# Kernel optimization log

Hardware: AMD Instinct MI355X
Metric: run time of the kernel (lower is better)

## Reference

```python
import jax, jax.numpy as jnp
import numpy as np

N = 2048      # total nodes across all graphs
G = 16        # number of graphs
IN = 16       # input_dim
D = 256       # hidden_dim (d_model)
NH = 8        # num_heads
HD = D // NH  # head_dim
FF = 4 * D    # dim_feedforward
L = 4         # num_layers
LAT = 32      # latent_dim
BH = D // 2   # beta_head hidden
LN_EPS = 1e-5


def setup_inputs() -> dict:
    key = jax.random.key(0)
    ks = jax.random.split(key, 32)

    def w(k, shape, fan_in):
        return jax.random.normal(k, shape, jnp.float32) * (1.0 / np.sqrt(fan_in))

    inp = {
        "x": jax.random.normal(ks[0], (N, IN), jnp.float32),
        "coords": jax.random.normal(ks[1], (N, 3), jnp.float32),
        "batch": jnp.sort(jax.random.randint(ks[2], (N,), 0, G)).astype(jnp.int32),
        # input projection
        "Wi": w(ks[3], (IN, D), IN), "bi": jnp.zeros((D,), jnp.float32),
        # per-layer transformer params, stacked on leading layer dim
        "qkv_w": w(ks[4], (L, D, 3 * D), D), "qkv_b": jnp.zeros((L, 3 * D), jnp.float32),
        "out_w": w(ks[5], (L, D, D), D),     "out_b": jnp.zeros((L, D), jnp.float32),
        "ff1_w": w(ks[6], (L, D, FF), D),    "ff1_b": jnp.zeros((L, FF), jnp.float32),
        "ff2_w": w(ks[7], (L, FF, D), FF),   "ff2_b": jnp.zeros((L, D), jnp.float32),
        "ln1_s": jnp.ones((L, D), jnp.float32), "ln1_b": jnp.zeros((L, D), jnp.float32),
        "ln2_s": jnp.ones((L, D), jnp.float32), "ln2_b": jnp.zeros((L, D), jnp.float32),
        # heads
        "lat_w": w(ks[8], (D, LAT), D), "lat_b": jnp.zeros((LAT,), jnp.float32),
        "b1_w": w(ks[9], (D, BH), D),   "b1_b": jnp.zeros((BH,), jnp.float32),
        "b2_w": w(ks[10], (BH, 1), BH), "b2_b": jnp.zeros((1,), jnp.float32),
    }
    return inp


def _layer_norm(h, s, b):
    m = jnp.mean(h, axis=-1, keepdims=True)
    v = jnp.mean(jnp.square(h - m), axis=-1, keepdims=True)
    return (h - m) * jax.lax.rsqrt(v + LN_EPS) * s + b


def _forward(x, batch, Wi, bi, qkv_w, qkv_b, out_w, out_b, ff1_w, ff1_b,
             ff2_w, ff2_b, ln1_s, ln1_b, ln2_s, ln2_b, lat_w, lat_b,
             b1_w, b1_b, b2_w, b2_b):
    n = x.shape[0]
    h = x @ Wi + bi  # [N, D]
    # the per-graph python loop in torch == block-diagonal attention mask
    attn_bias = jnp.where(batch[:, None] == batch[None, :], 0.0, -1e9).astype(h.dtype)  # [N, N]
    scale = 1.0 / np.sqrt(HD)
    for l in range(L):
        qkv = h @ qkv_w[l] + qkv_b[l]                 # [N, 3D]
        q, k, v = jnp.split(qkv, 3, axis=-1)
        q = q.reshape(n, NH, HD)
        k = k.reshape(n, NH, HD)
        v = v.reshape(n, NH, HD)
        scores = jnp.einsum('nhd,mhd->hnm', q, k) * scale + attn_bias[None]  # [H, N, N]
        a = jax.nn.softmax(scores, axis=-1)
        o = jnp.einsum('hnm,mhd->nhd', a, v).reshape(n, D)
        o = o @ out_w[l] + out_b[l]
        h = _layer_norm(h + o, ln1_s[l], ln1_b[l])     # post-norm (torch default)
        f = jax.nn.relu(h @ ff1_w[l] + ff1_b[l]) @ ff2_w[l] + ff2_b[l]
        h = _layer_norm(h + f, ln2_s[l], ln2_b[l])
    lat = h @ lat_w + lat_b                            # [N, LAT]
    norm = jnp.maximum(jnp.linalg.norm(lat, axis=-1, keepdims=True), 1e-12)
    lat = lat / norm * np.sqrt(LAT)
    beta = jax.nn.sigmoid(jax.nn.relu(h @ b1_w + b1_b) @ b2_w + b2_b)  # [N, 1]
    beta = jnp.clip(beta, 1e-6, 1.0 - 1e-6)
    return beta, lat


def reference(x, coords, batch, Wi, bi, qkv_w, qkv_b, out_w, out_b,
              ff1_w, ff1_b, ff2_w, ff2_b, ln1_s, ln1_b, ln2_s, ln2_b,
              lat_w, lat_b, b1_w, b1_b, b2_w, b2_b):
    # coords is accepted (signature fidelity) but unused in the original forward
    del coords
    return _forward(x, batch, Wi, bi, qkv_w, qkv_b, out_w, out_b, ff1_w, ff1_b,
                    ff2_w, ff2_b, ln1_s, ln1_b, ln2_s, ln2_b, lat_w, lat_b,
                    b1_w, b1_b, b2_w, b2_b)
```

## Files before the change

kernel.cpp:

```cpp
#include <hip/hip_runtime.h>
#include <hip/hip_bf16.h>

typedef __attribute__((ext_vector_type(8))) short bf16x8;
typedef __attribute__((ext_vector_type(4))) float f32x4;

__device__ inline float wave_sum64(float v) {
#pragma unroll
  for (int m = 32; m >= 1; m >>= 1) v += __shfl_xor(v, m, 64);
  return v;
}
__device__ inline ushort f2bf(float f) {
  uint u = __float_as_uint(f);
  return (ushort)((u + 0x7FFFu + ((u >> 16) & 1u)) >> 16);
}

__global__ __launch_bounds__(256) void pack_inproj(
    const float* __restrict__ qkv_w, const float* __restrict__ out_w,
    const float* __restrict__ ff1_w, const float* __restrict__ ff2_w,
    const float* __restrict__ b1_w, const float* __restrict__ lat_w,
    short* __restrict__ qkv_t, short* __restrict__ out_t,
    short* __restrict__ ff1_t, short* __restrict__ ff2_t,
    short* __restrict__ b1_t, short* __restrict__ lat_t,
    const int* __restrict__ batch, int* __restrict__ starts, int* __restrict__ meta,
    const float* __restrict__ x, const float* __restrict__ Wi,
    const float* __restrict__ bi, float* __restrict__ h, short* __restrict__ hb) {
  int t = blockIdx.x;
  __shared__ float tile[32][33];

  if (t >= 3113) {
    const int row = t - 3113;
    const int j = threadIdx.x;
    float* xs = &tile[0][0];
    if (j < 16) xs[j] = x[(size_t)row * 16 + j];
    __syncthreads();
    float acc = bi[j];
#pragma unroll
    for (int k = 0; k < 16; ++k) acc += xs[k] * Wi[k * 256 + j];
    h[(size_t)row * 256 + j] = acc;
    hb[(size_t)row * 256 + j] = (short)f2bf(acc);
    return;
  }
  if (t == 3112) {
    for (int i = threadIdx.x; i < 2048; i += 256) {
      int b = batch[i];
      if (i == 0) {
        for (int g = 0; g <= b; ++g) starts[g] = 0;
      } else {
        int bp = batch[i - 1];
        for (int g = bp + 1; g <= b; ++g) starts[g] = i;
      }
      if (i == 2047) {
        for (int g = b + 1; g <= 16; ++g) starts[g] = 2048;
      }
    }
    __syncthreads();
    if (threadIdx.x == 0) {
      int nt = 0;
      for (int g = 0; g < 16; ++g) {
        const int js = starts[g], je = starts[g + 1];
        for (int q0 = js; q0 < je; q0 += 16) {
          meta[1 + nt * 3] = q0;
          meta[2 + nt * 3] = js;
          meta[3 + nt * 3] = je;
          ++nt;
        }
      }
      meta[0] = nt;
    }
    return;
  }
  const float* src;
  short* dst;
  int Kd, Nd, rem;
  if (t < 768) {
    int l = t / 192; rem = t % 192; Kd = 256; Nd = 768;
    src = qkv_w + (size_t)l * Kd * Nd; dst = qkv_t + (size_t)l * Nd * Kd;
  } else if (t < 1024) {
    t -= 768; int l = t / 64; rem = t % 64; Kd = 256; Nd = 256;
    src = out_w + (size_t)l * Kd * Nd; dst = out_t + (size_t)l * Nd * Kd;
  } else if (t < 2048) {
    t -= 1024; int l = t / 256; rem = t % 256; Kd = 256; Nd = 1024;
    src = ff1_w + (size_t)l * Kd * Nd; dst = ff1_t + (size_t)l * Nd * Kd;
  } else if (t < 3072) {
    t -= 2048; int l = t / 256; rem = t % 256; Kd = 1024; Nd = 256;
    src = ff2_w + (size_t)l * Kd * Nd; dst = ff2_t + (size_t)l * Nd * Kd;
  } else if (t < 3104) {
    rem = t - 3072; Kd = 256; Nd = 128; src = b1_w; dst = b1_t;
  } else {
    rem = t - 3104; Kd = 256; Nd = 32; src = lat_w; dst = lat_t;
  }
  const int ntn = Nd / 32;
  const int kt = rem / ntn, nt = rem % ntn;
  const int tx = threadIdx.x & 31, ty = threadIdx.x >> 5;
#pragma unroll
  for (int r = 0; r < 4; ++r) {
    int k = kt * 32 + ty + r * 8;
    tile[ty + r * 8][tx] = src[(size_t)k * Nd + nt * 32 + tx];
  }
  __syncthreads();
#pragma unroll
  for (int r = 0; r < 4; ++r) {
    int n = nt * 32 + ty + r * 8;
    dst[(size_t)n * Kd + kt * 32 + tx] = (short)f2bf(tile[tx][ty + r * 8]);
  }
}

template <int ACT, int P, int VT>
__global__ __launch_bounds__(256) void gemm_bf16(
    const short* __restrict__ A, const short* __restrict__ Bt,
    const float* __restrict__ bias, float* __restrict__ Cf, short* __restrict__ Cb,
    short* __restrict__ vtg, int M, int N, int K, int kpb) {
  __shared__ short As[64 * 128];
  __shared__ short Bs[64 * 128];

  const int t = threadIdx.x;
  const int bm = blockIdx.y, bn = blockIdx.x, bz = blockIdx.z;
  const int srow = t >> 2, sq = t & 3;
  const int lane = t & 63, wid = t >> 6;
  const int wr = wid >> 1, wc = wid & 1;
  const int fr = lane & 15, fs = lane >> 4;
  const int rx = srow & 7;

  f32x4 acc[2][2];
#pragma unroll
  for (int m = 0; m < 2; ++m)
#pragma unroll
    for (int n = 0; n < 2; ++n) acc[m][n] = (f32x4){0.f, 0.f, 0.f, 0.f};

  const int kbase = bz * kpb;
  const short* ap = A + (size_t)(bm * 64 + srow) * K + kbase;
  const int ng = bn * 64 + srow;
  const short* bp = Bt + (size_t)ng * K + kbase;
  const int ar0 = wr * 32 + fr, ar1 = ar0 + 16;
  const int bc0 = wc * 32 + fr, bc1 = bc0 + 16;

  for (int k0 = 0; k0 < kpb; k0 += 128) {
    bf16x8 av[4], bv[4];
#pragma unroll
    for (int i = 0; i < 4; ++i) av[i] = *(const bf16x8*)(ap + k0 + (sq * 4 + i) * 8);
    if (ng < N) {
#pragma unroll
      for (int i = 0; i < 4; ++i) bv[i] = *(const bf16x8*)(bp + k0 + (sq * 4 + i) * 8);
    } else {
#pragma unroll
      for (int i = 0; i < 4; ++i) bv[i] = (bf16x8){0, 0, 0, 0, 0, 0, 0, 0};
    }
    __syncthreads();
#pragma unroll
    for (int i = 0; i < 4; ++i) {
      const int s = sq * 4 + i;
      *(bf16x8*)(As + srow * 128 + ((s ^ rx) * 8)) = av[i];
      *(bf16x8*)(Bs + srow * 128 + ((s ^ rx) * 8)) = bv[i];
    }
    __syncthreads();
#pragma unroll
    for (int ks = 0; ks < 4; ++ks) {
      const int u = ks * 4 + fs;
      bf16x8 a0 = *(const bf16x8*)(As + ar0 * 128 + ((u ^ (ar0 & 7)) * 8));
      bf16x8 a1 = *(const bf16x8*)(As + ar1 * 128 + ((u ^ (ar1 & 7)) * 8));
      bf16x8 b0 = *(const bf16x8*)(Bs + bc0 * 128 + ((u ^ (bc0 & 7)) * 8));
      bf16x8 b1 = *(const bf16x8*)(Bs + bc1 * 128 + ((u ^ (bc1 & 7)) * 8));
      acc[0][0] = __builtin_amdgcn_mfma_f32_16x16x32_bf16(a0, b0, acc[0][0], 0, 0, 0);
      acc[0][1] = __builtin_amdgcn_mfma_f32_16x16x32_bf16(a0, b1, acc[0][1], 0, 0, 0);
      acc[1][0] = __builtin_amdgcn_mfma_f32_16x16x32_bf16(a1, b0, acc[1][0], 0, 0, 0);
      acc[1][1] = __builtin_amdgcn_mfma_f32_16x16x32_bf16(a1, b1, acc[1][1], 0, 0, 0);
    }
  }

  if (P == 0) {
    if (!(VT && bn >= 8)) {
#pragma unroll
      for (int n = 0; n < 2; ++n) {
        const int col = bn * 64 + wc * 32 + n * 16 + fr;
        if (col < N) {
          const float bvv = bias[col];
#pragma unroll
          for (int m = 0; m < 2; ++m) {
            const int rbase = bm * 64 + wr * 32 + m * 16 + fs * 4;
#pragma unroll
            for (int j = 0; j < 4; ++j) {
              float v = acc[m][n][j] + bvv;
              if (ACT == 1) v = fmaxf(v, 0.f);
              Cb[(size_t)(rbase + j) * N + col] = (short)f2bf(v);
            }
          }
        }
      }
    }
    if (VT && bn >= 8) {
      short* tr = As;
      __syncthreads();
#pragma unroll
      for (int n = 0; n < 2; ++n) {
        const int c = wc * 32 + n * 16 + fr;
        const float bvv = bias[bn * 64 + c];
#pragma unroll
        for (int m = 0; m < 2; ++m)
#pragma unroll
          for (int j = 0; j < 4; ++j) {
            const int r = wr * 32 + m * 16 + fs * 4 + j;
            tr[c * 68 + r] = (short)f2bf(acc[m][n][j] + bvv);
          }
      }
      __syncthreads();
      const int tx = t & 63, ty = t >> 6;
      const int d0 = bn * 64 - 512, rb = bm * 64;
#pragma unroll
      for (int r = 0; r < 16; ++r) {
        const int d = ty * 16 + r;
        vtg[(size_t)(d0 + d) * 2048 + rb + tx] = tr[d * 68 + tx];
      }
    }
  } else {
#pragma unroll
    for (int n = 0; n < 2; ++n) {
      const int col = bn * 64 + wc * 32 + n * 16 + fr;
      const float bvv = (bz == 0) ? bias[col] : 0.f;
#pragma unroll
      for (int m = 0; m < 2; ++m) {
        const int rbase = bm * 64 + wr * 32 + m * 16 + fs * 4;
#pragma unroll
        for (int j = 0; j < 4; ++j) {
          Cf[(size_t)(bz * M + rbase + j) * N + col] = acc[m][n][j] + bvv;
        }
      }
    }
  }
}

__global__ __launch_bounds__(256) void attn_op(
    const short* __restrict__ qkv, const short* __restrict__ vtg,
    const int* __restrict__ meta, const short* __restrict__ out_t,
    float* __restrict__ tmp) {
  __shared__ short Ot[4][16][40];
  const int w = threadIdx.x >> 6;
  const int wid = blockIdx.x * 4 + w;
  const int tile = wid >> 3, h = wid & 7;
  const bool active = (tile < meta[0]);
  const int lane = threadIdx.x & 63;
  const int fr = lane & 15, fs = lane >> 4;
  const int q0 = active ? meta[1 + tile * 3] : 0;
  const int js = active ? meta[2 + tile * 3] : 0;
  const int je = active ? meta[3 + tile * 3] : 0;
  const int jbase = js & ~15;
  const int njt = active ? ((je - jbase + 15) >> 4) : 0;
  const float scale = 0.17677669529663687f;

  const int qrow = min(q0 + fr, 2047);
  const bf16x8 qf = *(const bf16x8*)(qkv + (size_t)qrow * 768 + h * 32 + fs * 8);
  const int jeq = (q0 + fr < je) ? je : 0;

  f32x4 s[16];
#pragma unroll
  for (int jt = 0; jt < 16; ++jt)
    s[jt] = (f32x4){-3.0e38f, -3.0e38f, -3.0e38f, -3.0e38f};

#pragma unroll
  for (int jt = 0; jt < 16; ++jt) {
    if (jt < njt) {
      const int krow = min(jbase + jt * 16 + fr, 2047);
      const bf16x8 kf = *(const bf16x8*)(qkv + (size_t)krow * 768 + 256 + h * 32 + fs * 8);
      s[jt] = __builtin_amdgcn_mfma_f32_16x16x32_bf16(
          kf, qf, (f32x4){0.f, 0.f, 0.f, 0.f}, 0, 0, 0);
    }
  }
  float mx = -3.0e38f;
#pragma unroll
  for (int jt = 0; jt < 16; ++jt) {
    if (jt < njt) {
#pragma unroll
      for (int jj = 0; jj < 4; ++jj) {
        const int j = jbase + jt * 16 + fs * 4 + jj;
        const bool valid = (j >= js) && (j < jeq);
        s[jt][jj] = valid ? s[jt][jj] * scale : -3.0e38f;
        mx = fmaxf(mx, s[jt][jj]);
      }
    }
  }
  mx = fmaxf(mx, __shfl_xor(mx, 16, 64));
  mx = fmaxf(mx, __shfl_xor(mx, 32, 64));
  float l = 0.f;
#pragma unroll
  for (int jt = 0; jt < 16; ++jt) {
#pragma unroll
    for (int jj = 0; jj < 4; ++jj) {
      const float p = __expf(s[jt][jj] - mx);
      s[jt][jj] = p;
      l += p;
    }
  }
  l += __shfl_xor(l, 16, 64);
  l += __shfl_xor(l, 32, 64);

  f32x4 oa[2];
  oa[0] = (f32x4){0.f, 0.f, 0.f, 0.f};
  oa[1] = (f32x4){0.f, 0.f, 0.f, 0.f};
#pragma unroll
  for (int p2 = 0; p2 < 8; ++p2) {
    if (p2 * 2 < njt) {
      bf16x8 pa;
      pa[0] = (short)f2bf(s[p2 * 2][0]);     pa[1] = (short)f2bf(s[p2 * 2][1]);
      pa[2] = (short)f2bf(s[p2 * 2][2]);     pa[3] = (short)f2bf(s[p2 * 2][3]);
      pa[4] = (short)f2bf(s[p2 * 2 + 1][0]); pa[5] = (short)f2bf(s[p2 * 2 + 1][1]);
      pa[6] = (short)f2bf(s[p2 * 2 + 1][2]); pa[7] = (short)f2bf(s[p2 * 2 + 1][3]);
      const int jb0 = min(jbase + p2 * 32 + fs * 4, 2044);
      const int jb1 = min(jbase + p2 * 32 + 16 + fs * 4, 2044);
#pragma unroll
      for (int nt = 0; nt < 2; ++nt) {
        const short* vrow = vtg + (size_t)(h * 32 + nt * 16 + fr) * 2048;
        const short4 v0 = *(const short4*)(vrow + jb0);
        const short4 v1 = *(const short4*)(vrow + jb1);
        bf16x8 vf;
        vf[0] = v0.x; vf[1] = v0.y; vf[2] = v0.z; vf[3] = v0.w;
        vf[4] = v1.x; vf[5] = v1.y; vf[6] = v1.z; vf[7] = v1.w;
        oa[nt] = __builtin_amdgcn_mfma_f32_16x16x32_bf16(pa, vf, oa[nt], 0, 0, 0);
      }
    }
  }

#pragma unroll
  for (int jj = 0; jj < 4; ++jj) {
    const float lq = __shfl(l, fs * 4 + jj, 64);
    const float inv = (lq > 0.f) ? (1.f / lq) : 0.f;
    const int q = fs * 4 + jj;
    Ot[w][q][fr] = (short)f2bf(oa[0][jj] * inv);
    Ot[w][q][16 + fr] = (short)f2bf(oa[1][jj] * inv);
  }
  __syncthreads();

  const bf16x8 afrag = *(const bf16x8*)&Ot[w][fr][fs * 8];
  const short* wbase = out_t + (size_t)fr * 256 + h * 32 + fs * 8;
  if (active) {
#pragma unroll
    for (int nt = 0; nt < 16; ++nt) {
      const bf16x8 bfrag = *(const bf16x8*)(wbase + (size_t)nt * 16 * 256);
      f32x4 c = __builtin_amdgcn_mfma_f32_16x16x32_bf16(
          afrag, bfrag, (f32x4){0.f, 0.f, 0.f, 0.f}, 0, 0, 0);
#pragma unroll
      for (int jj = 0; jj < 4; ++jj) {
        const int node = q0 + fs * 4 + jj;
        if (node < je) {
          tmp[((size_t)h * 2048 + node) * 256 + nt * 16 + fr] = c[jj];
        }
      }
    }
  }
}

template <int P, bool BIAS>
__global__ __launch_bounds__(256) void ln_kernel(
    const float* __restrict__ base, const float* __restrict__ delta,
    const float* __restrict__ cbias, const float* __restrict__ s,
    const float* __restrict__ b, float* __restrict__ outf, short* __restrict__ outb) {
  const int row = blockIdx.x * 4 + (threadIdx.x >> 6);
  const int lane = threadIdx.x & 63;
  float4 v = *(const float4*)(base + (size_t)row * 256 + lane * 4);
  if (BIAS) {
    const float4 cb = *(const float4*)(cbias + lane * 4);
    v.x += cb.x; v.y += cb.y; v.z += cb.z; v.w += cb.w;
  }
#pragma unroll
  for (int p = 0; p < P; ++p) {
    const float4 xb = *(const float4*)(delta + (size_t)(p * 2048 + row) * 256 + lane * 4);
    v.x += xb.x; v.y += xb.y; v.z += xb.z; v.w += xb.w;
  }
  float sum = wave_sum64(v.x + v.y + v.z + v.w);
  const float mean = sum * (1.f / 256.f);
  float4 d = make_float4(v.x - mean, v.y - mean, v.z - mean, v.w - mean);
  float sq = wave_sum64(d.x * d.x + d.y * d.y + d.z * d.z + d.w * d.w);
  const float rs = rsqrtf(sq * (1.f / 256.f) + 1e-5f);
  const float4 sv = *(const float4*)(s + lane * 4);
  const float4 bv = *(const float4*)(b + lane * 4);
  float4 o = make_float4(d.x * rs * sv.x + bv.x, d.y * rs * sv.y + bv.y,
                         d.z * rs * sv.z + bv.z, d.w * rs * sv.w + bv.w);
  *(float4*)(outf + (size_t)row * 256 + lane * 4) = o;
  short4 ob;
  ob.x = (short)f2bf(o.x); ob.y = (short)f2bf(o.y);
  ob.z = (short)f2bf(o.z); ob.w = (short)f2bf(o.w);
  *(short4*)(outb + (size_t)row * 256 + lane * 4) = ob;
}

__global__ __launch_bounds__(256) void heads_kernel(
    const short* __restrict__ A, const short* __restrict__ lat_t,
    const float* __restrict__ lat_b, float* __restrict__ lat_out,
    const short* __restrict__ b1_t, const float* __restrict__ b1b,
    const float* __restrict__ w2, const float* __restrict__ b2b,
    float* __restrict__ beta) {
  __shared__ short smem[64 * 128 * 2];
  const int t = threadIdx.x;
  const int lane = t & 63, w = t >> 6;
  const int fr = lane & 15, fs = lane >> 4;

  if (blockIdx.x < 32) {
    short* As = smem;
    short* Bs = smem + 64 * 128;
    const int bm = blockIdx.x;
    const int srow = t >> 2, sq = t & 3;
    const int rx = srow & 7;
    f32x4 acc[2];
    acc[0] = (f32x4){0.f, 0.f, 0.f, 0.f};
    acc[1] = (f32x4){0.f, 0.f, 0.f, 0.f};
    const short* ap = A + (size_t)(bm * 64 + srow) * 256;
    const short* bp = lat_t + (size_t)srow * 256;
    const int ar = w * 16 + fr;
    for (int k0 = 0; k0 < 256; k0 += 128) {
      bf16x8 av[4], bv[4];
#pragma unroll
      for (int i = 0; i < 4; ++i) av[i] = *(const bf16x8*)(ap + k0 + (sq * 4 + i) * 8);
      if (srow < 32) {
#pragma unroll
        for (int i = 0; i < 4; ++i) bv[i] = *(const bf16x8*)(bp + k0 + (sq * 4 + i) * 8);
      } else {
#pragma unroll
        for (int i = 0; i < 4; ++i) bv[i] = (bf16x8){0, 0, 0, 0, 0, 0, 0, 0};
      }
      __syncthreads();
#pragma unroll
      for (int i = 0; i < 4; ++i) {
        const int s = sq * 4 + i;
        *(bf16x8*)(As + srow * 128 + ((s ^ rx) * 8)) = av[i];
        *(bf16x8*)(Bs + srow * 128 + ((s ^ rx) * 8)) = bv[i];
      }
      __syncthreads();
#pragma unroll
      for (int ks = 0; ks < 4; ++ks) {
        const int u = ks * 4 + fs;
        bf16x8 a0 = *(const bf16x8*)(As + ar * 128 + ((u ^ (ar & 7)) * 8));
        bf16x8 b0 = *(const bf16x8*)(Bs + fr * 128 + ((u ^ (fr & 7)) * 8));
        bf16x8 b1 = *(const bf16x8*)(Bs + (16 + fr) * 128 + ((u ^ ((16 + fr) & 7)) * 8));
        acc[0] = __builtin_amdgcn_mfma_f32_16x16x32_bf16(a0, b0, acc[0], 0, 0, 0);
        acc[1] = __builtin_amdgcn_mfma_f32_16x16x32_bf16(a0, b1, acc[1], 0, 0, 0);
      }
    }
    const float b0v = lat_b[fr], b1v = lat_b[16 + fr];
#pragma unroll
    for (int j = 0; j < 4; ++j) {
      const int row = bm * 64 + w * 16 + fs * 4 + j;
      float v0 = acc[0][j] + b0v;
      float v1 = acc[1][j] + b1v;
      float ss = v0 * v0 + v1 * v1;
      ss += __shfl_xor(ss, 1, 64);
      ss += __shfl_xor(ss, 2, 64);
      ss += __shfl_xor(ss, 4, 64);
      ss += __shfl_xor(ss, 8, 64);
      const float inv = 5.656854249492381f / fmaxf(sqrtf(ss), 1e-12f);
      lat_out[(size_t)row * 32 + fr] = v0 * inv;
      lat_out[(size_t)row * 32 + 16 + fr] = v1 * inv;
    }
  } else {
    float* red = (float*)smem;
    const int rb = (blockIdx.x - 32) * 16;
    f32x4 acc[2];
    acc[0] = (f32x4){0.f, 0.f, 0.f, 0.f};
    acc[1] = (f32x4){0.f, 0.f, 0.f, 0.f};
    const short* ap = A + (size_t)(rb + fr) * 256;
    const short* bp = b1_t + (size_t)(w * 32 + fr) * 256;
    for (int k0 = 0; k0 < 256; k0 += 32) {
      const bf16x8 af = *(const bf16x8*)(ap + k0 + fs * 8);
#pragma unroll
      for (int n = 0; n < 2; ++n) {
        const bf16x8 bf = *(const bf16x8*)(bp + (size_t)n * 16 * 256 + k0 + fs * 8);
        acc[n] = __builtin_amdgcn_mfma_f32_16x16x32_bf16(af, bf, acc[n], 0, 0, 0);
      }
    }
    const int c0 = w * 32 + fr, c1 = c0 + 16;
    const float b0 = b1b[c0], b1 = b1b[c1];
    const float w0 = w2[c0], w1 = w2[c1];
    float part[4];
#pragma unroll
    for (int j = 0; j < 4; ++j) {
      const float d0 = fmaxf(acc[0][j] + b0, 0.f);
      const float d1 = fmaxf(acc[1][j] + b1, 0.f);
      part[j] = d0 * w0 + d1 * w1;
#pragma unroll
      for (int m = 1; m <= 8; m <<= 1) part[j] += __shfl_xor(part[j], m, 64);
    }
    if (fr == 0) {
#pragma unroll
      for (int j = 0; j < 4; ++j) red[w * 16 + fs * 4 + j] = part[j];
    }
    __syncthreads();
    if (t < 16) {
      const float S = red[t] + red[16 + t] + red[32 + t] + red[48 + t] + b2b[0];
      float sgm = 1.f / (1.f + __expf(-S));
      sgm = fminf(fmaxf(sgm, 1e-6f), 1.f - 1e-6f);
      beta[rb + t] = sgm;
    }
  }
}

extern "C" void kernel_launch(void* const* d_in, const int* in_sizes, int n_in,
                              void* d_out, int out_size, void* d_ws, size_t ws_size,
                              hipStream_t stream) {
  const int N = 2048, D = 256, FF = 1024, L = 4;

  const float* x     = (const float*)d_in[0];
  const int*   batch = (const int*)d_in[2];
  const float* Wi    = (const float*)d_in[3];
  const float* bi    = (const float*)d_in[4];
  const float* qkv_w = (const float*)d_in[5];
  const float* qkv_b = (const float*)d_in[6];
  const float* out_w = (const float*)d_in[7];
  const float* out_b = (const float*)d_in[8];
  const float* ff1_w = (const float*)d_in[9];
  const float* ff1_b = (const float*)d_in[10];
  const float* ff2_w = (const float*)d_in[11];
  const float* ff2_b = (const float*)d_in[12];
  const float* ln1_s = (const float*)d_in[13];
  const float* ln1_b = (const float*)d_in[14];
  const float* ln2_s = (const float*)d_in[15];
  const float* ln2_b = (const float*)d_in[16];
  const float* lat_w = (const float*)d_in[17];
  const float* lat_b = (const float*)d_in[18];
  const float* b1_w  = (const float*)d_in[19];
  const float* b1_b  = (const float*)d_in[20];
  const float* b2_w  = (const float*)d_in[21];
  const float* b2_b  = (const float*)d_in[22];

  float* ws = (float*)d_ws;
  float* h      = ws;
  float* tmp    = h + (size_t)N * D;
  int*  starts  = (int*)(tmp + (size_t)8 * N * D);
  int*  meta    = starts + 32;
  short* hb     = (short*)(meta + 448);
  short* qkvb   = hb + (size_t)N * D;
  short* ffb    = qkvb + (size_t)N * 3 * D;
  short* vtg    = ffb + (size_t)N * FF;
  short* qkv_t  = vtg + (size_t)256 * 2048;
  short* out_t  = qkv_t + (size_t)L * 768 * 256;
  short* ff1_t  = out_t + (size_t)L * 256 * 256;
  short* ff2_t  = ff1_t + (size_t)L * 1024 * 256;
  short* b1_t   = ff2_t + (size_t)L * 256 * 1024;
  short* lat_t  = b1_t + (size_t)128 * 256;

  float* beta_out = (float*)d_out;
  float* lat_out  = beta_out + N;

  pack_inproj<<<3113 + 2048, 256, 0, stream>>>(
      qkv_w, out_w, ff1_w, ff2_w, b1_w, lat_w,
      qkv_t, out_t, ff1_t, ff2_t, b1_t, lat_t,
      batch, starts, meta, x, Wi, bi, h, hb);

  for (int l = 0; l < L; ++l) {
    gemm_bf16<0, 0, 1><<<dim3(12, 32, 1), 256, 0, stream>>>(
        hb, qkv_t + (size_t)l * 768 * 256, qkv_b + (size_t)l * 768,
        nullptr, qkvb, vtg, N, 768, 256, 256);
    attn_op<<<288, 256, 0, stream>>>(qkvb, vtg, meta,
                                     out_t + (size_t)l * 256 * 256, tmp);
    ln_kernel<8, true><<<N / 4, 256, 0, stream>>>(
        h, tmp, out_b + (size_t)l * 256, ln1_s + (size_t)l * D,
        ln1_b + (size_t)l * D, h, hb);
    gemm_bf16<1, 0, 0><<<dim3(16, 32, 1), 256, 0, stream>>>(
        hb, ff1_t + (size_t)l * FF * 256, ff1_b + (size_t)l * FF,
        nullptr, ffb, nullptr, N, FF, 256, 256);
    gemm_bf16<0, 4, 0><<<dim3(4, 32, 4), 256, 0, stream>>>(
        ffb, ff2_t + (size_t)l * 256 * FF, ff2_b + (size_t)l * 256,
        tmp, nullptr, nullptr, N, 256, 1024, 256);
    ln_kernel<4, false><<<N / 4, 256, 0, stream>>>(
        h, tmp, nullptr, ln2_s + (size_t)l * D, ln2_b + (size_t)l * D, h, hb);
  }

  heads_kernel<<<160, 256, 0, stream>>>(hb, lat_t, lat_b, lat_out,
                                        b1_t, b1_b, b2_w, b2_b, beta_out);
}
```

Baseline: 215.0 us.

## Fuse attention, output projection, residual and LayerNorm into one per-tile kernel

Each block now handles one query tile with all 8 heads, one per wave. The per-head outputs are shared through LDS so the output projection becomes a full K=256 reduction inside the block, each wave producing 32 output columns. The bias, residual add and LayerNorm are then applied in place using a cross-wave reduction in shared memory. This removes the 8-way partial-sum writes to tmp and the separate ln_kernel launch that read them back, cutting global traffic and one launch per layer. In exchange there are fewer, larger blocks (144 of 512 threads), and the variance is computed as E[x²]−mean² instead of the two-pass form, which is slightly less numerically stable.

```diff
diff --git a/kernel.cpp b/kernel.cpp
--- a/kernel.cpp
+++ b/kernel.cpp
@@ -228,14 +228,15 @@
   }
 }
 
-__global__ __launch_bounds__(256) void attn_op(
+__global__ __launch_bounds__(512) void attn_fused(
     const short* __restrict__ qkv, const short* __restrict__ vtg,
     const int* __restrict__ meta, const short* __restrict__ out_t,
-    float* __restrict__ tmp) {
-  __shared__ short Ot[4][16][40];
+    const float* __restrict__ outb, const float* __restrict__ lns,
+    const float* __restrict__ lnb, float* __restrict__ h, short* __restrict__ hb) {
+  __shared__ short Ot[8][16][40];
+  __shared__ float redS[8][16], redQ[8][16];
   const int w = threadIdx.x >> 6;
-  const int wid = blockIdx.x * 4 + w;
-  const int tile = wid >> 3, h = wid & 7;
+  const int tile = blockIdx.x;
   const bool active = (tile < meta[0]);
   const int lane = threadIdx.x & 63;
   const int fr = lane & 15, fs = lane >> 4;
@@ -247,7 +248,7 @@
   const float scale = 0.17677669529663687f;
 
   const int qrow = min(q0 + fr, 2047);
-  const bf16x8 qf = *(const bf16x8*)(qkv + (size_t)qrow * 768 + h * 32 + fs * 8);
+  const bf16x8 qf = *(const bf16x8*)(qkv + (size_t)qrow * 768 + w * 32 + fs * 8);
   const int jeq = (q0 + fr < je) ? je : 0;
 
   f32x4 s[16];
@@ -259,7 +260,7 @@
   for (int jt = 0; jt < 16; ++jt) {
     if (jt < njt) {
       const int krow = min(jbase + jt * 16 + fr, 2047);
-      const bf16x8 kf = *(const bf16x8*)(qkv + (size_t)krow * 768 + 256 + h * 32 + fs * 8);
+      const bf16x8 kf = *(const bf16x8*)(qkv + (size_t)krow * 768 + 256 + w * 32 + fs * 8);
       s[jt] = __builtin_amdgcn_mfma_f32_16x16x32_bf16(
           kf, qf, (f32x4){0.f, 0.f, 0.f, 0.f}, 0, 0, 0);
     }
@@ -307,7 +308,7 @@
       const int jb1 = min(jbase + p2 * 32 + 16 + fs * 4, 2044);
 #pragma unroll
       for (int nt = 0; nt < 2; ++nt) {
-        const short* vrow = vtg + (size_t)(h * 32 + nt * 16 + fr) * 2048;
+        const short* vrow = vtg + (size_t)(w * 32 + nt * 16 + fr) * 2048;
         const short4 v0 = *(const short4*)(vrow + jb0);
         const short4 v1 = *(const short4*)(vrow + jb1);
         bf16x8 vf;
@@ -328,37 +329,78 @@
   }
   __syncthreads();
 
-  const bf16x8 afrag = *(const bf16x8*)&Ot[w][fr][fs * 8];
-  const short* wbase = out_t + (size_t)fr * 256 + h * 32 + fs * 8;
-  if (active) {
-#pragma unroll
-    for (int nt = 0; nt < 16; ++nt) {
-      const bf16x8 bfrag = *(const bf16x8*)(wbase + (size_t)nt * 16 * 256);
-      f32x4 c = __builtin_amdgcn_mfma_f32_16x16x32_bf16(
-          afrag, bfrag, (f32x4){0.f, 0.f, 0.f, 0.f}, 0, 0, 0);
-#pragma unroll
-      for (int jj = 0; jj < 4; ++jj) {
-        const int node = q0 + fs * 4 + jj;
-        if (node < je) {
-          tmp[((size_t)h * 2048 + node) * 256 + nt * 16 + fr] = c[jj];
-        }
-      }
-    }
-  }
-}
-
-template <int P, bool BIAS>
+  f32x4 acc2[2];
+  acc2[0] = (f32x4){0.f, 0.f, 0.f, 0.f};
+  acc2[1] = (f32x4){0.f, 0.f, 0.f, 0.f};
+#pragma unroll
+  for (int ks = 0; ks < 8; ++ks) {
+    const bf16x8 afrag = *(const bf16x8*)&Ot[ks][fr][fs * 8];
+#pragma unroll
+    for (int nt2 = 0; nt2 < 2; ++nt2) {
+      const int col_row = (w * 2 + nt2) * 16 + fr;
+      const bf16x8 bfrag =
+          *(const bf16x8*)(out_t + (size_t)col_row * 256 + ks * 32 + fs * 8);
+      acc2[nt2] = __builtin_amdgcn_mfma_f32_16x16x32_bf16(afrag, bfrag, acc2[nt2], 0, 0, 0);
+    }
+  }
+
+  float d[2][4], ps[4], pq[4];
+#pragma unroll
+  for (int jj = 0; jj < 4; ++jj) {
+    const int node = q0 + fs * 4 + jj;
+    const int noder = min(node, 2047);
+#pragma unroll
+    for (int nt2 = 0; nt2 < 2; ++nt2) {
+      const int col = w * 32 + nt2 * 16 + fr;
+      d[nt2][jj] = acc2[nt2][jj] + outb[col] + h[(size_t)noder * 256 + col];
+    }
+    ps[jj] = d[0][jj] + d[1][jj];
+    pq[jj] = d[0][jj] * d[0][jj] + d[1][jj] * d[1][jj];
+#pragma unroll
+    for (int m = 1; m <= 8; m <<= 1) {
+      ps[jj] += __shfl_xor(ps[jj], m, 64);
+      pq[jj] += __shfl_xor(pq[jj], m, 64);
+    }
+  }
+  if (fr == 0) {
+#pragma unroll
+    for (int jj = 0; jj < 4; ++jj) {
+      redS[w][fs * 4 + jj] = ps[jj];
+      redQ[w][fs * 4 + jj] = pq[jj];
+    }
+  }
+  __syncthreads();
+
+#pragma unroll
+  for (int jj = 0; jj < 4; ++jj) {
+    const int row = fs * 4 + jj;
+    float S = 0.f, Q = 0.f;
+#pragma unroll
+    for (int ww = 0; ww < 8; ++ww) { S += redS[ww][row]; Q += redQ[ww][row]; }
+    const float mean = S * (1.f / 256.f);
+    const float var = Q * (1.f / 256.f) - mean * mean;
+    const float rs = rsqrtf(var + 1e-5f);
+    const int node = q0 + row;
+    if (active && node < je) {
+#pragma unroll
+      for (int nt2 = 0; nt2 < 2; ++nt2) {
+        const int col = w * 32 + nt2 * 16 + fr;
+        const float o = (d[nt2][jj] - mean) * rs * lns[col] + lnb[col];
+        h[(size_t)node * 256 + col] = o;
+        hb[(size_t)node * 256 + col] = (short)f2bf(o);
+      }
+    }
+  }
+}
+
+template <int P>
 __global__ __launch_bounds__(256) void ln_kernel(
     const float* __restrict__ base, const float* __restrict__ delta,
-    const float* __restrict__ cbias, const float* __restrict__ s,
-    const float* __restrict__ b, float* __restrict__ outf, short* __restrict__ outb) {
+    const float* __restrict__ s, const float* __restrict__ b,
+    float* __restrict__ outf, short* __restrict__ outb) {
   const int row = blockIdx.x * 4 + (threadIdx.x >> 6);
   const int lane = threadIdx.x & 63;
   float4 v = *(const float4*)(base + (size_t)row * 256 + lane * 4);
-  if (BIAS) {
-    const float4 cb = *(const float4*)(cbias + lane * 4);
-    v.x += cb.x; v.y += cb.y; v.z += cb.z; v.w += cb.w;
-  }
 #pragma unroll
   for (int p = 0; p < P; ++p) {
     const float4 xb = *(const float4*)(delta + (size_t)(p * 2048 + row) * 256 + lane * 4);
@@ -520,7 +562,7 @@
   float* ws = (float*)d_ws;
   float* h      = ws;
   float* tmp    = h + (size_t)N * D;
-  int*  starts  = (int*)(tmp + (size_t)8 * N * D);
+  int*  starts  = (int*)(tmp + (size_t)4 * N * D);
   int*  meta    = starts + 32;
   short* hb     = (short*)(meta + 448);
   short* qkvb   = hb + (size_t)N * D;
@@ -545,19 +587,17 @@
     gemm_bf16<0, 0, 1><<<dim3(12, 32, 1), 256, 0, stream>>>(
         hb, qkv_t + (size_t)l * 768 * 256, qkv_b + (size_t)l * 768,
         nullptr, qkvb, vtg, N, 768, 256, 256);
-    attn_op<<<288, 256, 0, stream>>>(qkvb, vtg, meta,
-                                     out_t + (size_t)l * 256 * 256, tmp);
-    ln_kernel<8, true><<<N / 4, 256, 0, stream>>>(
-        h, tmp, out_b + (size_t)l * 256, ln1_s + (size_t)l * D,
-        ln1_b + (size_t)l * D, h, hb);
+    attn_fused<<<144, 512, 0, stream>>>(
+        qkvb, vtg, meta, out_t + (size_t)l * 256 * 256, out_b + (size_t)l * 256,
+        ln1_s + (size_t)l * D, ln1_b + (size_t)l * D, h, hb);
     gemm_bf16<1, 0, 0><<<dim3(16, 32, 1), 256, 0, stream>>>(
         hb, ff1_t + (size_t)l * FF * 256, ff1_b + (size_t)l * FF,
         nullptr, ffb, nullptr, N, FF, 256, 256);
     gemm_bf16<0, 4, 0><<<dim3(4, 32, 4), 256, 0, stream>>>(
         ffb, ff2_t + (size_t)l * 256 * FF, ff2_b + (size_t)l * 256,
         tmp, nullptr, nullptr, N, 256, 1024, 256);
-    ln_kernel<4, false><<<N / 4, 256, 0, stream>>>(
-        h, tmp, nullptr, ln2_s + (size_t)l * D, ln2_b + (size_t)l * D, h, hb);
+    ln_kernel<4><<<N / 4, 256, 0, stream>>>(
+        h, tmp, ln2_s + (size_t)l * D, ln2_b + (size_t)l * D, h, hb);
   }
 
   heads_kernel<<<160, 256, 0, stream>>>(hb, lat_t, lat_b, lat_out,
```

Measured after the change: 190.5 us (median of 2 runs). -11.4%, faster.
